# Kernel optimization log

Hardware: AMD Instinct MI355X
Metric: run time of the kernel (lower is better)

The kernel has to match this reference:

```python
import jax, jax.numpy as jnp
import numpy as np
from jax import lax

B, C, L, K = 8, 256, 4096, 65
PAD = K // 2  # torch: int(kernel.shape[-1] / 2) = 32 -> same-length output for odd K


def depthwise_corr(x, k):
    """Depthwise cross-correlation (torch conv1d semantics, no kernel flip).
    x: [B, C, L] float32, k: [K] float32 (same kernel shared by all channels,
    matching kernel.repeat(seq_len, 1)). Returns [B, C, L]."""
    w = jnp.broadcast_to(k.reshape(1, 1, K), (C, 1, K))  # [C, 1, K]
    return lax.conv_general_dilated(
        x, w, window_strides=(1,), padding=[(PAD, PAD)],
        dimension_numbers=("NCH", "OIH", "NCH"), feature_group_count=C)


def setup_inputs() -> dict:
    key = jax.random.key(0)
    k1, k2, k3 = jax.random.split(key, 3)
    return {
        "x": jax.random.normal(k1, (B, C, L), dtype=jnp.float32),
        "kernel_real": jax.random.normal(k2, (K,), dtype=jnp.float32),
        "kernel_imag": jax.random.normal(k3, (K,), dtype=jnp.float32),
        "weights_mag": jnp.ones((1, C, 1), dtype=jnp.float32),
        "weights_angle": jnp.ones((1, C, 1), dtype=jnp.float32),
    }


def reference(x, kernel_real, kernel_imag, weights_mag, weights_angle):
    # mf_coeffs = conj(kernel) -> weight = kernel_real - 1j*kernel_imag.
    # Input x is real (imag=0 after .to(complex64)), so complex conv splits
    # into two real depthwise correlations.
    yr = depthwise_corr(x, kernel_real)            # [B, C, L]
    yi = -depthwise_corr(x, kernel_imag)           # [B, C, L]
    y = lax.complex(yr, yi)                        # complex64 [B, C, L]

    # torch.std over dims (1,2), unbiased (correction=1), complex -> real std
    mean = jnp.mean(y, axis=(1, 2), keepdims=True)
    n = C * L
    var = jnp.sum(jnp.abs(y - mean) ** 2, axis=(1, 2), keepdims=True) / (n - 1)
    y = y / jnp.sqrt(var)                          # real std broadcasts over complex

    # weights_mag * y * exp(-1j * weights_angle)
    phase = lax.complex(jnp.cos(weights_angle), -jnp.sin(weights_angle))  # [1, C, 1]
    y = weights_mag * y * phase

    # FFT over the channel dim (dim=-2), then fftshift on that dim
    return jnp.fft.fftshift(jnp.fft.fft(y, axis=-2), axes=-2)
```

## Files before the change

kernel.cpp:

```cpp
#include <hip/hip_runtime.h>
#include <math.h>

#define NB 8
#define NC 256
#define NL 4096
#define NK 65

__device__ float g_stats[NB * 4];

__global__ void zero_stats_kernel() {
    if (threadIdx.x < NB * 4) g_stats[threadIdx.x] = 0.0f;
}


#define LOAD16(W, off)                                                      \
    {                                                                       \
        const int g0_ = l0 + (off);                                         \
        if (g0_ >= 0 && g0_ + 16 <= NL) {         \
            _Pragma("unroll")                                               \
            for (int q = 0; q < 4; ++q) {                                   \
                const float4 v_ = *(const float4*)(xr + g0_ + 4 * q);       \
                W[4*q+0] = v_.x; W[4*q+1] = v_.y;                           \
                W[4*q+2] = v_.z; W[4*q+3] = v_.w;                           \
            }                                                               \
        } else {                                                            \
            _Pragma("unroll")                                               \
            for (int q = 0; q < 16; ++q) {                                  \
                const int g_ = g0_ + q;                                     \
                W[q] = (g_ >= 0 && g_ < NL) ? xr[g_] : 0.0f;                \
            }                                                               \
        }                                                                   \
    }

#define CHUNK16(Lo, Hi, tb)                                                 \
    {                                                                       \
        _Pragma("unroll")                                                   \
        for (int j2 = 0; j2 < 16; ++j2) {                                   \
            const float kr_ = kre[(tb) + j2];        \
            const float ki_ = kim[(tb) + j2];                               \
            _Pragma("unroll")                                               \
            for (int i = 0; i < 16; ++i) {                                  \
                const int wi_ = i + j2;                                     \
                const float xv_ = (wi_ < 16) ? Lo[wi_] : Hi[wi_ - 16];      \
                sr[i] = fmaf(xv_, kr_, sr[i]);                              \
                si[i] = fmaf(xv_, ki_, si[i]);                              \
            }                                                               \
        }                                                                   \
    }

__global__ __launch_bounds__(256) void fused_conv_fft_kernel(
    const float* __restrict__ x,
    const float* __restrict__ kre,
    const float* __restrict__ kim,
    const float* __restrict__ wmag,
    const float* __restrict__ wang,
    float* __restrict__ out,
    int out_size)
{
    __shared__ __align__(16) float4 lbuf4[NC * 9];
    __shared__ float twr[NC], twi[NC];
    __shared__ float red[12];

    const int t = threadIdx.x;
    const int b = blockIdx.x & 7;
    const int l0 = (blockIdx.x >> 3) << 4;

    {
        float ang = (float)t * 0.024543692606170260f;
        float s, c;
        sincosf(ang, &s, &c);
        twr[t] = c; twi[t] = -s;
    }
    float sw, cw;
    sincosf(wang[t], &sw, &cw);
    const float wm = wmag[t];
    const float wgr =  wm * cw;
    const float wgi = -wm * sw;

    const float* xr = x + (size_t)b * NC * NL + (size_t)t * NL;
    const bool interleaved = (out_size >= 2 * NB * NC * NL);

    float sr[16], si[16];
    #pragma unroll
    for (int i = 0; i < 16; ++i) { sr[i] = 0.0f; si[i] = 0.0f; }

    float A[16], B[16];
    LOAD16(A, -32);
    LOAD16(B, -16);
    CHUNK16(A, B, 0);
    LOAD16(A, 0);
    CHUNK16(B, A, 16);
    LOAD16(B, 16);
    CHUNK16(A, B, 32);
    LOAD16(A, 32);
    CHUNK16(B, A, 48);
    {
        const float kr_ = kre[64];
        const float ki_ = kim[64];
        #pragma unroll
        for (int i = 0; i < 16; ++i) {
            sr[i] = fmaf(A[i], kr_, sr[i]);
            si[i] = fmaf(A[i], ki_, si[i]);
        }
    }

    float tsr = 0.0f, tsi = 0.0f, tsq = 0.0f;
    #pragma unroll
    for (int i = 0; i < 16; ++i) {
        tsr += sr[i];
        tsi -= si[i];
        tsq = fmaf(sr[i], sr[i], tsq);
        tsq = fmaf(si[i], si[i], tsq);
    }

    #pragma unroll
    for (int k = 0; k < 8; ++k) {
        float4 o;
        o.x = sr[2*k]   * wgr + si[2*k]   * wgi;
        o.y = sr[2*k]   * wgi - si[2*k]   * wgr;
        o.z = sr[2*k+1] * wgr + si[2*k+1] * wgi;
        o.w = sr[2*k+1] * wgi - si[2*k+1] * wgr;
        lbuf4[t * 9 + k] = o;
    }
    __syncthreads();

    #pragma unroll
    for (int s = 0; s < 4; ++s) {
        const int shift = 2 * s;
        const int q = 64 >> shift;
        #pragma unroll
        for (int it = 0; it < 2; ++it) {
            int task = it * 256 + t;
            int lpp = task & 7;
            int m = task >> 3;
            int j = m & (q - 1);
            int blk = m >> (6 - shift);
            int base2 = blk << (8 - shift);
            int e = j << shift;

            int ca = base2 + j;
            float4 a0 = lbuf4[ca*9 + lpp];
            float4 a1 = lbuf4[(ca + q)*9 + lpp];
            float4 a2 = lbuf4[(ca + 2*q)*9 + lpp];
            float4 a3 = lbuf4[(ca + 3*q)*9 + lpp];

            float w1r = twr[e],   w1i = twi[e];
            float w2r = twr[2*e], w2i = twi[2*e];
            float w3r = twr[3*e], w3i = twi[3*e];

            float4 b0, b1, b2, b3;
            {
                float t0r = a0.x + a2.x, t0i = a0.y + a2.y;
                float t1r = a0.x - a2.x, t1i = a0.y - a2.y;
                float t2r = a1.x + a3.x, t2i = a1.y + a3.y;
                float t3r = a1.x - a3.x, t3i = a1.y - a3.y;
                b0.x = t0r + t2r;       b0.y = t0i + t2i;
                float b2r = t0r - t2r,  b2i = t0i - t2i;
                float b1r = t1r + t3i,  b1i = t1i - t3r;
                float b3r = t1r - t3i,  b3i = t1i + t3r;
                b1.x = b1r*w1r - b1i*w1i;  b1.y = b1r*w1i + b1i*w1r;
                b2.x = b2r*w2r - b2i*w2i;  b2.y = b2r*w2i + b2i*w2r;
                b3.x = b3r*w3r - b3i*w3i;  b3.y = b3r*w3i + b3i*w3r;
            }
            {
                float t0r = a0.z + a2.z, t0i = a0.w + a2.w;
                float t1r = a0.z - a2.z, t1i = a0.w - a2.w;
                float t2r = a1.z + a3.z, t2i = a1.w + a3.w;
                float t3r = a1.z - a3.z, t3i = a1.w - a3.w;
                b0.z = t0r + t2r;       b0.w = t0i + t2i;
                float b2r = t0r - t2r,  b2i = t0i - t2i;
                float b1r = t1r + t3i,  b1i = t1i - t3r;
                float b3r = t1r - t3i,  b3i = t1i + t3r;
                b1.z = b1r*w1r - b1i*w1i;  b1.w = b1r*w1i + b1i*w1r;
                b2.z = b2r*w2r - b2i*w2i;  b2.w = b2r*w2i + b2i*w2r;
                b3.z = b3r*w3r - b3i*w3i;  b3.w = b3r*w3i + b3i*w3r;
            }
            lbuf4[ca*9 + lpp]         = b0;
            lbuf4[(ca + q)*9 + lpp]   = b1;
            lbuf4[(ca + 2*q)*9 + lpp] = b2;
            lbuf4[(ca + 3*q)*9 + lpp] = b3;
        }
        __syncthreads();
    }

    #pragma unroll
    for (int it = 0; it < 8; ++it) {
        int task = it * 256 + t;
        int lpp = task & 7;
        int pp = task >> 3;
        float4 v = lbuf4[pp*9 + lpp];
        int k = ((pp & 3) << 6) | (((pp >> 2) & 3) << 4)
              | (((pp >> 4) & 3) << 2) | ((pp >> 6) & 3);
        int cout = k ^ 128;
        if (interleaved) {
            size_t fi = 2 * ((size_t)(b * NC + cout) * NL + l0) + 4 * lpp;
            if (fi + 4 <= (size_t)out_size) *(float4*)(out + fi) = v;
        } else {
            size_t fi = (size_t)(b * NC + cout) * NL + l0 + 2 * lpp;
            if (fi + 2 <= (size_t)out_size) {
                float2 o2; o2.x = v.x; o2.y = v.z;
                *(float2*)(out + fi) = o2;
            }
        }
    }

    #pragma unroll
    for (int off = 32; off > 0; off >>= 1) {
        tsr += __shfl_down(tsr, off);
        tsi += __shfl_down(tsi, off);
        tsq += __shfl_down(tsq, off);
    }
    const int lane = t & 63, wv = t >> 6;
    if (lane == 0) { red[wv*3+0] = tsr; red[wv*3+1] = tsi; red[wv*3+2] = tsq; }
    __syncthreads();
    if (t == 0) {
        float a0 = 0.0f, a1 = 0.0f, a2 = 0.0f;
        for (int i = 0; i < 4; ++i) { a0 += red[i*3]; a1 += red[i*3+1]; a2 += red[i*3+2]; }
        atomicAdd(&g_stats[b*4+0], a0);
        atomicAdd(&g_stats[b*4+1], a1);
        atomicAdd(&g_stats[b*4+2], a2);
    }
}

__global__ __launch_bounds__(256) void scale_out_kernel(
    float* __restrict__ out, int out_size)
{
    __shared__ float sinv[NB];
    const int t = threadIdx.x;
    if (t < NB) {
        float sr = g_stats[t*4+0], si = g_stats[t*4+1], sq = g_stats[t*4+2];
        const float n = (float)(NC * NL);
        float var = (sq - (sr*sr + si*si)/n) / (n - 1.0f);
        sinv[t] = rsqrtf(var);
    }
    __syncthreads();

    const int chunk = out_size >> 3;
    const bool p2 = (chunk & (chunk - 1)) == 0;
    const int lb = 31 - __clz(chunk);
    const int n4 = out_size >> 2;
    float4* o4 = (float4*)out;
    for (int i4 = blockIdx.x * blockDim.x + t; i4 < n4;
         i4 += gridDim.x * blockDim.x) {
        int fi = i4 << 2;
        int bidx = p2 ? (fi >> lb) : (fi / chunk);
        float inv = sinv[bidx];
        float4 v = o4[i4];
        v.x *= inv; v.y *= inv; v.z *= inv; v.w *= inv;
        o4[i4] = v;
    }
    int tail0 = n4 << 2;
    int ti = tail0 + blockIdx.x * blockDim.x + t;
    if (ti < out_size) {
        int bidx = p2 ? (ti >> lb) : (ti / chunk);
        out[ti] *= sinv[bidx];
    }
}

extern "C" void kernel_launch(void* const* d_in, const int* in_sizes, int n_in,
                              void* d_out, int out_size, void* d_ws, size_t ws_size,
                              hipStream_t stream)
{
    const float* x   = (const float*)d_in[0];
    const float* kre = (const float*)d_in[1];
    const float* kim = (const float*)d_in[2];
    const float* wm  = (const float*)d_in[3];
    const float* wa  = (const float*)d_in[4];
    float* out = (float*)d_out;
    (void)d_ws; (void)ws_size;

    zero_stats_kernel<<<1, 64, 0, stream>>>();
    fused_conv_fft_kernel<<<NB * (NL / 16), 256, 0, stream>>>(x, kre, kim, wm, wa,
                                                              out, out_size);
    scale_out_kernel<<<2048, 256, 0, stream>>>(out, out_size);
}
```

Measured before the change: 151.6 us.

## Fuse conv, FFT and normalization into one cooperative kernel with grid sync

Replaces the three-kernel pipeline (zero stats, conv+FFT with atomics, global rescale pass) with a single cooperative kernel of 1024 blocks. Each block processes two 16-column tiles, writes per-block partial statistics, grid-syncs, then reduces the partials and scales its outputs before writing. The first tile is held in registers (planar case) or re-read from global (interleaved case), and the second tile stays in shared memory. This removes the separate full read-modify-write pass over the output and two launches. In exchange the kernel needs all blocks co-resident, adds a grid barrier, and raises register pressure. It falls back to the old path if the cooperative launch fails.

```diff
diff --git a/kernel.cpp b/kernel.cpp
--- a/kernel.cpp
+++ b/kernel.cpp
@@ -1,17 +1,17 @@
 #include <hip/hip_runtime.h>
+#include <hip/hip_cooperative_groups.h>
 #include <math.h>
+
+namespace cg = cooperative_groups;
 
 #define NB 8
 #define NC 256
 #define NL 4096
 #define NK 65
-
+#define NST 128
+
+__device__ float4 g_part[NB * NST];
 __device__ float g_stats[NB * 4];
-
-__global__ void zero_stats_kernel() {
-    if (threadIdx.x < NB * 4) g_stats[threadIdx.x] = 0.0f;
-}
-
 
 #define LOAD16(W, off)                                                      \
     {                                                                       \
@@ -48,37 +48,14 @@
         }                                                                   \
     }
 
-__global__ __launch_bounds__(256) void fused_conv_fft_kernel(
-    const float* __restrict__ x,
-    const float* __restrict__ kre,
-    const float* __restrict__ kim,
-    const float* __restrict__ wmag,
-    const float* __restrict__ wang,
-    float* __restrict__ out,
-    int out_size)
+__device__ __forceinline__ void conv_fft_tile(
+    const float* __restrict__ xr,
+    const float* __restrict__ kre, const float* __restrict__ kim,
+    float wgr, float wgi, int l0,
+    float4* lbuf4, const float* twr, const float* twi,
+    float& tsr_a, float& tsi_a, float& tsq_a)
 {
-    __shared__ __align__(16) float4 lbuf4[NC * 9];
-    __shared__ float twr[NC], twi[NC];
-    __shared__ float red[12];
-
     const int t = threadIdx.x;
-    const int b = blockIdx.x & 7;
-    const int l0 = (blockIdx.x >> 3) << 4;
-
-    {
-        float ang = (float)t * 0.024543692606170260f;
-        float s, c;
-        sincosf(ang, &s, &c);
-        twr[t] = c; twi[t] = -s;
-    }
-    float sw, cw;
-    sincosf(wang[t], &sw, &cw);
-    const float wm = wmag[t];
-    const float wgr =  wm * cw;
-    const float wgi = -wm * sw;
-
-    const float* xr = x + (size_t)b * NC * NL + (size_t)t * NL;
-    const bool interleaved = (out_size >= 2 * NB * NC * NL);
 
     float sr[16], si[16];
     #pragma unroll
@@ -104,15 +81,15 @@
         }
     }
 
-    float tsr = 0.0f, tsi = 0.0f, tsq = 0.0f;
     #pragma unroll
     for (int i = 0; i < 16; ++i) {
-        tsr += sr[i];
-        tsi -= si[i];
-        tsq = fmaf(sr[i], sr[i], tsq);
-        tsq = fmaf(si[i], si[i], tsq);
-    }
-
+        tsr_a += sr[i];
+        tsi_a -= si[i];
+        tsq_a = fmaf(sr[i], sr[i], tsq_a);
+        tsq_a = fmaf(si[i], si[i], tsq_a);
+    }
+
+    __syncthreads();
     #pragma unroll
     for (int k = 0; k < 8; ++k) {
         float4 o;
@@ -182,16 +159,205 @@
         }
         __syncthreads();
     }
+}
+
+__device__ __forceinline__ int digitrev_shift(int pp) {
+    int k = ((pp & 3) << 6) | (((pp >> 2) & 3) << 4)
+          | (((pp >> 4) & 3) << 2) | ((pp >> 6) & 3);
+    return k ^ 128;
+}
+
+__global__ __launch_bounds__(256, 4) void fused_all_kernel(
+    const float* __restrict__ x,
+    const float* __restrict__ kre,
+    const float* __restrict__ kim,
+    const float* __restrict__ wmag,
+    const float* __restrict__ wang,
+    float* __restrict__ out,
+    int out_size)
+{
+    __shared__ __align__(16) float4 lbuf4[NC * 9];
+    __shared__ float twr[NC], twi[NC];
+    __shared__ float red[12];
+
+    const int t = threadIdx.x;
+    const int b = blockIdx.x & 7;
+    const int st = blockIdx.x >> 3;
+    const int l0A = st << 5;
+    const int l0B = l0A + 16;
+
+    {
+        float ang = (float)t * 0.024543692606170260f;
+        float s, c;
+        sincosf(ang, &s, &c);
+        twr[t] = c; twi[t] = -s;
+    }
+    float sw, cw;
+    sincosf(wang[t], &sw, &cw);
+    const float wm = wmag[t];
+    const float wgr =  wm * cw;
+    const float wgi = -wm * sw;
+
+    const float* xr = x + (size_t)b * NC * NL + (size_t)t * NL;
+    const bool interleaved = (out_size >= 2 * NB * NC * NL);
+
+    float tsr = 0.0f, tsi = 0.0f, tsq = 0.0f;
+
+    conv_fft_tile(xr, kre, kim, wgr, wgi, l0A, lbuf4, twr, twi, tsr, tsi, tsq);
+
+    float2 va2[8];
+    if (!interleaved) {
+        #pragma unroll
+        for (int it = 0; it < 8; ++it) {
+            int task = it * 256 + t;
+            int lpp = task & 7, pp = task >> 3;
+            float4 v = lbuf4[pp * 9 + lpp];
+            va2[it].x = v.x; va2[it].y = v.z;
+        }
+    } else {
+        #pragma unroll
+        for (int it = 0; it < 8; ++it) {
+            int task = it * 256 + t;
+            int lpp = task & 7, pp = task >> 3;
+            float4 v = lbuf4[pp * 9 + lpp];
+            int cout = digitrev_shift(pp);
+            size_t fi = 2 * ((size_t)(b * NC + cout) * NL + l0A) + 4 * lpp;
+            if (fi + 4 <= (size_t)out_size) *(float4*)(out + fi) = v;
+        }
+    }
+
+    conv_fft_tile(xr, kre, kim, wgr, wgi, l0B, lbuf4, twr, twi, tsr, tsi, tsq);
+
+    #pragma unroll
+    for (int off = 32; off > 0; off >>= 1) {
+        tsr += __shfl_down(tsr, off);
+        tsi += __shfl_down(tsi, off);
+        tsq += __shfl_down(tsq, off);
+    }
+    const int lane = t & 63, wv = t >> 6;
+    if (lane == 0) { red[wv*3+0] = tsr; red[wv*3+1] = tsi; red[wv*3+2] = tsq; }
+    __syncthreads();
+    if (t == 0) {
+        float a0 = 0.0f, a1 = 0.0f, a2 = 0.0f;
+        for (int i = 0; i < 4; ++i) { a0 += red[i*3]; a1 += red[i*3+1]; a2 += red[i*3+2]; }
+        g_part[b * NST + st] = make_float4(a0, a1, a2, 0.0f);
+    }
+
+    cg::this_grid().sync();
+
+    float psr = 0.0f, psi = 0.0f, psq = 0.0f;
+    if (t < NST) {
+        float4 p = g_part[b * NST + t];
+        psr = p.x; psi = p.y; psq = p.z;
+    }
+    #pragma unroll
+    for (int off = 32; off > 0; off >>= 1) {
+        psr += __shfl_down(psr, off);
+        psi += __shfl_down(psi, off);
+        psq += __shfl_down(psq, off);
+    }
+    if (wv < 2 && lane == 0) { red[wv*3+0] = psr; red[wv*3+1] = psi; red[wv*3+2] = psq; }
+    __syncthreads();
+    if (t == 0) {
+        float a0 = red[0] + red[3], a1 = red[1] + red[4], a2 = red[2] + red[5];
+        const float n = (float)(NC * NL);
+        float var = (a2 - (a0*a0 + a1*a1)/n) / (n - 1.0f);
+        red[0] = rsqrtf(var);
+    }
+    __syncthreads();
+    const float inv = red[0];
 
     #pragma unroll
     for (int it = 0; it < 8; ++it) {
         int task = it * 256 + t;
-        int lpp = task & 7;
-        int pp = task >> 3;
-        float4 v = lbuf4[pp*9 + lpp];
-        int k = ((pp & 3) << 6) | (((pp >> 2) & 3) << 4)
-              | (((pp >> 4) & 3) << 2) | ((pp >> 6) & 3);
-        int cout = k ^ 128;
+        int lpp = task & 7, pp = task >> 3;
+        float4 v = lbuf4[pp * 9 + lpp];
+        int cout = digitrev_shift(pp);
+        if (interleaved) {
+            v.x *= inv; v.y *= inv; v.z *= inv; v.w *= inv;
+            size_t fi = 2 * ((size_t)(b * NC + cout) * NL + l0B) + 4 * lpp;
+            if (fi + 4 <= (size_t)out_size) *(float4*)(out + fi) = v;
+        } else {
+            size_t fi = (size_t)(b * NC + cout) * NL + l0B + 2 * lpp;
+            if (fi + 2 <= (size_t)out_size) {
+                float2 o2; o2.x = v.x * inv; o2.y = v.z * inv;
+                *(float2*)(out + fi) = o2;
+            }
+        }
+    }
+    if (!interleaved) {
+        #pragma unroll
+        for (int it = 0; it < 8; ++it) {
+            int task = it * 256 + t;
+            int lpp = task & 7, pp = task >> 3;
+            int cout = digitrev_shift(pp);
+            size_t fi = (size_t)(b * NC + cout) * NL + l0A + 2 * lpp;
+            if (fi + 2 <= (size_t)out_size) {
+                float2 o2; o2.x = va2[it].x * inv; o2.y = va2[it].y * inv;
+                *(float2*)(out + fi) = o2;
+            }
+        }
+    } else {
+        #pragma unroll
+        for (int it = 0; it < 8; ++it) {
+            int task = it * 256 + t;
+            int lpp = task & 7, pp = task >> 3;
+            int cout = digitrev_shift(pp);
+            size_t fi = 2 * ((size_t)(b * NC + cout) * NL + l0A) + 4 * lpp;
+            if (fi + 4 <= (size_t)out_size) {
+                float4 v = *(const float4*)(out + fi);
+                v.x *= inv; v.y *= inv; v.z *= inv; v.w *= inv;
+                *(float4*)(out + fi) = v;
+            }
+        }
+    }
+}
+
+__global__ void zero_stats_kernel() {
+    if (threadIdx.x < NB * 4) g_stats[threadIdx.x] = 0.0f;
+}
+
+__global__ __launch_bounds__(256) void fused_conv_fft_kernel(
+    const float* __restrict__ x,
+    const float* __restrict__ kre,
+    const float* __restrict__ kim,
+    const float* __restrict__ wmag,
+    const float* __restrict__ wang,
+    float* __restrict__ out,
+    int out_size)
+{
+    __shared__ __align__(16) float4 lbuf4[NC * 9];
+    __shared__ float twr[NC], twi[NC];
+    __shared__ float red[12];
+
+    const int t = threadIdx.x;
+    const int b = blockIdx.x & 7;
+    const int l0 = (blockIdx.x >> 3) << 4;
+
+    {
+        float ang = (float)t * 0.024543692606170260f;
+        float s, c;
+        sincosf(ang, &s, &c);
+        twr[t] = c; twi[t] = -s;
+    }
+    float sw, cw;
+    sincosf(wang[t], &sw, &cw);
+    const float wm = wmag[t];
+    const float wgr =  wm * cw;
+    const float wgi = -wm * sw;
+
+    const float* xr = x + (size_t)b * NC * NL + (size_t)t * NL;
+    const bool interleaved = (out_size >= 2 * NB * NC * NL);
+
+    float tsr = 0.0f, tsi = 0.0f, tsq = 0.0f;
+    conv_fft_tile(xr, kre, kim, wgr, wgi, l0, lbuf4, twr, twi, tsr, tsi, tsq);
+
+    #pragma unroll
+    for (int it = 0; it < 8; ++it) {
+        int task = it * 256 + t;
+        int lpp = task & 7, pp = task >> 3;
+        float4 v = lbuf4[pp * 9 + lpp];
+        int cout = digitrev_shift(pp);
         if (interleaved) {
             size_t fi = 2 * ((size_t)(b * NC + cout) * NL + l0) + 4 * lpp;
             if (fi + 4 <= (size_t)out_size) *(float4*)(out + fi) = v;
@@ -244,9 +410,9 @@
          i4 += gridDim.x * blockDim.x) {
         int fi = i4 << 2;
         int bidx = p2 ? (fi >> lb) : (fi / chunk);
-        float inv = sinv[bidx];
+        float invv = sinv[bidx];
         float4 v = o4[i4];
-        v.x *= inv; v.y *= inv; v.z *= inv; v.w *= inv;
+        v.x *= invv; v.y *= invv; v.z *= invv; v.w *= invv;
         o4[i4] = v;
     }
     int tail0 = n4 << 2;
@@ -269,8 +435,17 @@
     float* out = (float*)d_out;
     (void)d_ws; (void)ws_size;
 
-    zero_stats_kernel<<<1, 64, 0, stream>>>();
-    fused_conv_fft_kernel<<<NB * (NL / 16), 256, 0, stream>>>(x, kre, kim, wm, wa,
-                                                              out, out_size);
-    scale_out_kernel<<<2048, 256, 0, stream>>>(out, out_size);
-}
+    void* args[7] = { (void*)&x, (void*)&kre, (void*)&kim, (void*)&wm,
+                      (void*)&wa, (void*)&out, (void*)&out_size };
+    hipError_t e = hipLaunchCooperativeKernel(
+        (const void*)fused_all_kernel, dim3(NB * NST), dim3(256),
+        args, 0, stream);
+
+    if (e != hipSuccess) {
+        (void)hipGetLastError();
+        zero_stats_kernel<<<1, 64, 0, stream>>>();
+        fused_conv_fft_kernel<<<NB * (NL / 16), 256, 0, stream>>>(
+            x, kre, kim, wm, wa, out, out_size);
+        scale_out_kernel<<<2048, 256, 0, stream>>>(out, out_size);
+    }
+}
```

Measured after the change: 289.6 us. 1.91x slower.
